# Performance work log

Measured on AMD Instinct MI355X. Metric: run time of the kernel, lower is better.

Reference implementation:

```python
import jax, jax.numpy as jnp
import numpy as np


def setup_inputs() -> dict:
    key = jax.random.key(0)
    k1, k2 = jax.random.split(key)
    B, C, H, W, D = 4, 32, 256, 512, 48
    h1 = jax.random.normal(k1, (B, C, H, W), dtype=jnp.float32)
    cost = jax.random.normal(k2, (B, D, H, W), dtype=jnp.float32)
    return {"h1": h1, "cost": cost}


def reference(h1, cost):
    # g2[b,c,h,w] = sum_d cost[b,d,h,w] * stop_grad(h1)[b,c,h,w+d]  for w+d < W
    # (original torch code detaches h1, so grads only flow through cost)
    B, C, H, W = h1.shape
    D = cost.shape[1]
    h1d = jax.lax.stop_gradient(h1)
    w_idx = jnp.arange(W)

    # scan over disparity levels; each step does a masked roll + fused MAC,
    # never materializing the [B,C,D,H,W] shifted stack.
    cost_d_major = jnp.moveaxis(cost, 1, 0)  # [D,B,H,W]

    def step(acc, xd):
        d, c_d = xd  # c_d: [B,H,W]
        valid = (w_idx < (W - d)).astype(h1.dtype)  # [W]; zero beyond W-d
        shifted = jnp.roll(h1d, -d, axis=-1) * valid  # h1[..., w+d], zero-padded
        acc = acc + c_d[:, None, :, :] * shifted  # broadcast over C
        return acc, None

    g2, _ = jax.lax.scan(step, jnp.zeros_like(h1), (jnp.arange(D), cost_d_major))
    return g2
```

## Files before the change

### kernel.cpp

```cpp
#include <hip/hip_runtime.h>


#define BB 4
#define CC 32
#define HH 256
#define WW 512
#define DDISP 48
#define HW (HH * WW)
#define TW 256
#define WPAD 316
#define NT 512

__global__ __launch_bounds__(NT, 2)
void dense_warp_kernel(const float* __restrict__ h1,
                       const float* __restrict__ cost,
                       float* __restrict__ out)
{
    __shared__ float h1s[CC * WPAD];

    const int blk    = blockIdx.x;
    const int wside  = blk & 1;
    const int h      = (blk >> 1) & (HH - 1);
    const int b      = blk >> 9;
    const int wstart = wside * TW;
    const int tid    = threadIdx.x;

    {
        const float* src = h1 + ((size_t)b * CC * HH + (size_t)h) * WW;
        for (int idx = tid; idx < CC * 78; idx += NT) {
            int r    = idx / 78;
            int q    = idx - r * 78;
            int col  = q << 2;
            int wsrc = wstart + col;
            float4 v = make_float4(0.f, 0.f, 0.f, 0.f);
            if (wsrc < WW) v = *(const float4*)(src + (size_t)r * HW + wsrc);
            *(float4*)(&h1s[r * WPAD + col]) = v;
        }
    }
    __syncthreads();

    const int wg = tid & 31;
    const int cg = tid >> 5;
    const int w0 = wg << 3;
    const int c0 = cg << 1;

    float acc[2][8];
#pragma unroll
    for (int c = 0; c < 2; ++c)
#pragma unroll
        for (int j = 0; j < 8; ++j) acc[c][j] = 0.f;

    float win[2][12];
#pragma unroll
    for (int c = 0; c < 2; ++c) {
        const float* p = &h1s[(c0 + c) * WPAD + w0];
#pragma unroll
        for (int q = 0; q < 3; ++q) {
            float4 v = *(const float4*)(p + (q << 2));
            win[c][q * 4 + 0] = v.x; win[c][q * 4 + 1] = v.y;
            win[c][q * 4 + 2] = v.z; win[c][q * 4 + 3] = v.w;
        }
    }

    const float* costBase = cost + ((size_t)b * DDISP * HH + (size_t)h) * WW + wstart + w0;

#define GROUP(G, gexpr) do {                                                   \
    const int g_ = (gexpr);                                                    \
    _Pragma("unroll")                                                          \
    for (int dd = 0; dd < 4; ++dd) {                                           \
        const float* cp = costBase + (size_t)(4 * g_ + dd) * HW;               \
        float4 ca = *(const float4*)cp;                                        \
        float4 cbv = *(const float4*)(cp + 4);                                 \
        float c8[8] = {ca.x, ca.y, ca.z, ca.w, cbv.x, cbv.y, cbv.z, cbv.w};    \
        _Pragma("unroll")                                                      \
        for (int c = 0; c < 2; ++c) {                                          \
            _Pragma("unroll")                                                  \
            for (int j = 0; j < 8; ++j) {                                      \
                const int o = dd + j;                               \
                const int s = ((G) + (o >> 2)) % 3;                            \
                acc[c][j] += c8[j] * win[c][s * 4 + (o & 3)];                   \
            }                                                                  \
        }                                                                      \
    }                                                                          \
    _Pragma("unroll")                                                          \
    for (int c = 0; c < 2; ++c) {   \
        float4 v = *(const float4*)(&h1s[(c0 + c) * WPAD + w0 + 4 * g_ + 12]); \
        win[c][(G) * 4 + 0] = v.x; win[c][(G) * 4 + 1] = v.y;                  \
        win[c][(G) * 4 + 2] = v.z; win[c][(G) * 4 + 3] = v.w;                  \
    }                                                                          \
} while (0)

    for (int g3 = 0; g3 < 4; ++g3) {
        GROUP(0, g3 * 3 + 0);
        GROUP(1, g3 * 3 + 1);
        GROUP(2, g3 * 3 + 2);
    }
#undef GROUP

    float* outBase = out + ((size_t)b * CC * HH + (size_t)h) * WW + wstart + w0;
#pragma unroll
    for (int c = 0; c < 2; ++c) {
        float* op = outBase + (size_t)(c0 + c) * HW;
        *(float4*)op       = make_float4(acc[c][0], acc[c][1], acc[c][2], acc[c][3]);
        *(float4*)(op + 4) = make_float4(acc[c][4], acc[c][5], acc[c][6], acc[c][7]);
    }
}

extern "C" void kernel_launch(void* const* d_in, const int* in_sizes, int n_in,
                              void* d_out, int out_size, void* d_ws, size_t ws_size,
                              hipStream_t stream) {
    const float* h1   = (const float*)d_in[0];
    const float* cost = (const float*)d_in[1];
    float* out        = (float*)d_out;
    dim3 grid(BB * HH * 2);
    dense_warp_kernel<<<grid, NT, 0, stream>>>(h1, cost, out);
}
```

Before: 263.9 us.

## Retile thread work to 8 channels x 4 columns with 256-thread blocks

Each thread now computes 8 channels by 4 output columns instead of 2 channels by 8 columns, and block size drops from 512 to 256 threads with a higher occupancy hint. Each cost value loaded from global memory is reused across 8 channels instead of 2, which cuts redundant cost traffic. The shared-memory window becomes a two-slot ring of 8 floats per channel. The trade-off is more registers per thread (larger acc and win arrays), which could limit occupancy.

```diff
diff --git a/kernel.cpp b/kernel.cpp
--- a/kernel.cpp
+++ b/kernel.cpp
@@ -8,15 +8,15 @@
 #define DDISP 48
 #define HW (HH * WW)
 #define TW 256
-#define WPAD 316
-#define NT 512
+#define WROW 312
+#define NT 256
 
-__global__ __launch_bounds__(NT, 2)
+__global__ __launch_bounds__(NT, 4)
 void dense_warp_kernel(const float* __restrict__ h1,
                        const float* __restrict__ cost,
                        float* __restrict__ out)
 {
-    __shared__ float h1s[CC * WPAD];
+    __shared__ float h1s[CC * WROW];
 
     const int blk    = blockIdx.x;
     const int wside  = blk & 1;
@@ -34,75 +34,79 @@
             int wsrc = wstart + col;
             float4 v = make_float4(0.f, 0.f, 0.f, 0.f);
             if (wsrc < WW) v = *(const float4*)(src + (size_t)r * HW + wsrc);
-            *(float4*)(&h1s[r * WPAD + col]) = v;
+            *(float4*)(&h1s[r * WROW + col]) = v;
         }
     }
     __syncthreads();
 
-    const int wg = tid & 31;
-    const int cg = tid >> 5;
-    const int w0 = wg << 3;
-    const int c0 = cg << 1;
+    const int lane = tid & 63;
+    const int wid  = tid >> 6;
+    const int c0   = wid << 3;
+    const int w0   = lane << 2;
 
-    float acc[2][8];
+    float acc[8][4];
 #pragma unroll
-    for (int c = 0; c < 2; ++c)
+    for (int c = 0; c < 8; ++c)
 #pragma unroll
-        for (int j = 0; j < 8; ++j) acc[c][j] = 0.f;
+        for (int j = 0; j < 4; ++j) acc[c][j] = 0.f;
 
-    float win[2][12];
+    float win[8][8];
+    const float* lptr = &h1s[c0 * WROW + w0];
 #pragma unroll
-    for (int c = 0; c < 2; ++c) {
-        const float* p = &h1s[(c0 + c) * WPAD + w0];
-#pragma unroll
-        for (int q = 0; q < 3; ++q) {
-            float4 v = *(const float4*)(p + (q << 2));
-            win[c][q * 4 + 0] = v.x; win[c][q * 4 + 1] = v.y;
-            win[c][q * 4 + 2] = v.z; win[c][q * 4 + 3] = v.w;
-        }
+    for (int c = 0; c < 8; ++c) {
+        float4 q0 = *(const float4*)(lptr + c * WROW);
+        float4 q1 = *(const float4*)(lptr + c * WROW + 4);
+        win[c][0] = q0.x; win[c][1] = q0.y; win[c][2] = q0.z; win[c][3] = q0.w;
+        win[c][4] = q1.x; win[c][5] = q1.y; win[c][6] = q1.z; win[c][7] = q1.w;
     }
 
-    const float* costBase = cost + ((size_t)b * DDISP * HH + (size_t)h) * WW + wstart + w0;
+    const float* cp = cost + ((size_t)b * DDISP * HH + (size_t)h) * WW + wstart + w0;
 
-#define GROUP(G, gexpr) do {                                                   \
-    const int g_ = (gexpr);                                                    \
+    float cv[4][4];
+
+#define LOADC(gofs) do {                                                       \
     _Pragma("unroll")                                                          \
     for (int dd = 0; dd < 4; ++dd) {                                           \
-        const float* cp = costBase + (size_t)(4 * g_ + dd) * HW;               \
-        float4 ca = *(const float4*)cp;                                        \
-        float4 cbv = *(const float4*)(cp + 4);                                 \
-        float c8[8] = {ca.x, ca.y, ca.z, ca.w, cbv.x, cbv.y, cbv.z, cbv.w};    \
-        _Pragma("unroll")                                                      \
-        for (int c = 0; c < 2; ++c) {                                          \
-            _Pragma("unroll")                                                  \
-            for (int j = 0; j < 8; ++j) {                                      \
-                const int o = dd + j;                               \
-                const int s = ((G) + (o >> 2)) % 3;                            \
-                acc[c][j] += c8[j] * win[c][s * 4 + (o & 3)];                   \
-            }                                                                  \
-        }                                                                      \
-    }                                                                          \
-    _Pragma("unroll")                                                          \
-    for (int c = 0; c < 2; ++c) {   \
-        float4 v = *(const float4*)(&h1s[(c0 + c) * WPAD + w0 + 4 * g_ + 12]); \
-        win[c][(G) * 4 + 0] = v.x; win[c][(G) * 4 + 1] = v.y;                  \
-        win[c][(G) * 4 + 2] = v.z; win[c][(G) * 4 + 3] = v.w;                  \
+        float4 t = *(const float4*)(cp + (size_t)((gofs) + dd) * HW);          \
+        cv[dd][0] = t.x; cv[dd][1] = t.y; cv[dd][2] = t.z; cv[dd][3] = t.w;    \
     }                                                                          \
 } while (0)
 
-    for (int g3 = 0; g3 < 4; ++g3) {
-        GROUP(0, g3 * 3 + 0);
-        GROUP(1, g3 * 3 + 1);
-        GROUP(2, g3 * 3 + 2);
+#define DO_GROUP(P) do {                                                       \
+    _Pragma("unroll")                                                          \
+    for (int c = 0; c < 8; ++c) {                                              \
+        _Pragma("unroll")                                                      \
+        for (int dd = 0; dd < 4; ++dd) {                                       \
+            _Pragma("unroll")                                                  \
+            for (int j = 0; j < 4; ++j) {                                      \
+                const int o    = dd + j;                             \
+                const int slot = ((P) + (o >> 2)) & 1;                         \
+                acc[c][j] += cv[dd][j] * win[c][slot * 4 + (o & 3)];           \
+            }                                                                  \
+        }                                                                      \
+                        \
+        float4 t = *(const float4*)(lptr + c * WROW + 8);                      \
+        win[c][(P) * 4 + 0] = t.x; win[c][(P) * 4 + 1] = t.y;                  \
+        win[c][(P) * 4 + 2] = t.z; win[c][(P) * 4 + 3] = t.w;                  \
+    }                                                                          \
+    lptr += 4;                                                                 \
+} while (0)
+
+    for (int ig = 0; ig < 6; ++ig) {
+        LOADC(0);
+        DO_GROUP(0);
+        LOADC(4);
+        DO_GROUP(1);
+        cp += (size_t)8 * HW;
     }
-#undef GROUP
+#undef LOADC
+#undef DO_GROUP
 
     float* outBase = out + ((size_t)b * CC * HH + (size_t)h) * WW + wstart + w0;
 #pragma unroll
-    for (int c = 0; c < 2; ++c) {
+    for (int c = 0; c < 8; ++c) {
         float* op = outBase + (size_t)(c0 + c) * HW;
-        *(float4*)op       = make_float4(acc[c][0], acc[c][1], acc[c][2], acc[c][3]);
-        *(float4*)(op + 4) = make_float4(acc[c][4], acc[c][5], acc[c][6], acc[c][7]);
+        *(float4*)op = make_float4(acc[c][0], acc[c][1], acc[c][2], acc[c][3]);
     }
 }
 
```

Measured after the change: 247.8 us. 6.1% less time.
